# Kernel optimization log

Hardware: AMD Instinct MI355X
Metric: run time of the kernel (lower is better)

## Reference

```python
import jax, jax.numpy as jnp
import numpy as np

N_NODES = 50000
SEQ = 12
CH = 128
BS = 4

def setup_inputs() -> dict:
    key = jax.random.key(0)
    k1, k2, k3, k4, k5 = jax.random.split(key, 5)
    x = jax.random.normal(k1, (BS, N_NODES, CH), dtype=jnp.float32)
    indices = jax.random.randint(k2, (N_NODES, SEQ), 0, N_NODES)
    # xavier-uniform-like init for per-node spiral weights [n_nodes, seq]
    bound = float(np.sqrt(6.0 / (N_NODES + SEQ)))
    weight = jax.random.uniform(k3, (N_NODES, SEQ), minval=-bound, maxval=bound, dtype=jnp.float32)
    gate_w = jax.random.normal(k4, (CH, CH), dtype=jnp.float32) * (1.0 / np.sqrt(CH))
    gate_b = jax.random.normal(k5, (CH,), dtype=jnp.float32) * 0.01
    return {"x": x, "indices": indices, "weight": weight, "gate_w": gate_w, "gate_b": gate_b}

def reference(x, indices, weight, gate_w, gate_b):
    # gate projection: [bs, n, ch]
    gate = jnp.einsum('bnc,dc->bnd', x, gate_w) + gate_b
    # gather spiral neighbors along node axis: [bs, n*s, ch] -> [bs, n, s, ch]
    gathered = jnp.take(x, indices.reshape(-1), axis=1)
    gathered = gathered.reshape(x.shape[0], indices.shape[0], indices.shape[1], x.shape[2])
    # per-node weighted reduction over spiral positions
    out = jnp.einsum('bvsf,vs->bvf', gathered, weight)
    return out * gate
```

## Files before the change

kernel.cpp:

```cpp
#include <hip/hip_runtime.h>
#include <hip/hip_bf16.h>

#define N_NODES 50000
#define SEQ 12
#define CH 128
#define BS 4
#define TILE 64
#define PAD_ROW 132

typedef short bf16x8 __attribute__((ext_vector_type(8)));
typedef float f32x4 __attribute__((ext_vector_type(4)));

__global__ __launch_bounds__(256) void convert_kernel(
    const float* __restrict__ x,
    const float* __restrict__ gate_w,
    __hip_bfloat16* __restrict__ xb,
    __hip_bfloat16* __restrict__ gwb)
{
    const size_t i = (size_t)blockIdx.x * 256 + threadIdx.x;
    const size_t n8 = (size_t)BS * N_NODES * CH / 8;
    if (i < n8) {
        float4 lo = *(const float4*)(x + i * 8);
        float4 hi = *(const float4*)(x + i * 8 + 4);
        union { bf16x8 v; __hip_bfloat16 h[8]; } o;
        o.h[0] = __float2bfloat16(lo.x); o.h[1] = __float2bfloat16(lo.y);
        o.h[2] = __float2bfloat16(lo.z); o.h[3] = __float2bfloat16(lo.w);
        o.h[4] = __float2bfloat16(hi.x); o.h[5] = __float2bfloat16(hi.y);
        o.h[6] = __float2bfloat16(hi.z); o.h[7] = __float2bfloat16(hi.w);
        *(bf16x8*)((unsigned short*)xb + i * 8) = o.v;
    }
    if (i < (size_t)CH * CH / 8) {
        float4 lo = *(const float4*)(gate_w + i * 8);
        float4 hi = *(const float4*)(gate_w + i * 8 + 4);
        union { bf16x8 v; __hip_bfloat16 h[8]; } o;
        o.h[0] = __float2bfloat16(lo.x); o.h[1] = __float2bfloat16(lo.y);
        o.h[2] = __float2bfloat16(lo.z); o.h[3] = __float2bfloat16(lo.w);
        o.h[4] = __float2bfloat16(hi.x); o.h[5] = __float2bfloat16(hi.y);
        o.h[6] = __float2bfloat16(hi.z); o.h[7] = __float2bfloat16(hi.w);
        *(bf16x8*)((unsigned short*)gwb + i * 8) = o.v;
    }
}

__global__ __launch_bounds__(256) void gated_spiral_bf16_kernel(
    const __hip_bfloat16* __restrict__ xb_all,
    const int* __restrict__ indices,
    const float* __restrict__ weight,
    const __hip_bfloat16* __restrict__ gwb,
    const float* __restrict__ gate_b,
    float* __restrict__ out)
{
    __shared__ float spiral[TILE * PAD_ROW];

    const int tile = blockIdx.x;
    const int b = blockIdx.y;
    const int tid = threadIdx.x;
    const int node0 = tile * TILE;

    const unsigned short* xbb = (const unsigned short*)xb_all + (size_t)b * N_NODES * CH;

    {
        const int v = node0 + (tid >> 2);
        const int vc = v < N_NODES ? v : N_NODES - 1;
        const int q = tid & 3;

        int   idxv[SEQ];
        float wf[SEQ];
        const int*   ip = indices + (size_t)vc * SEQ;
        const float* wp = weight  + (size_t)vc * SEQ;
        #pragma unroll
        for (int s = 0; s < SEQ; ++s) {
            int t = ip[s];
            t = t < 0 ? 0 : t;
            idxv[s] = t >= N_NODES ? N_NODES - 1 : t;
            wf[s] = wp[s];
        }

        float acc[32];
        #pragma unroll
        for (int i = 0; i < 32; ++i) acc[i] = 0.f;

        #pragma unroll
        for (int s = 0; s < SEQ; ++s) {
            const unsigned short* row = xbb + (size_t)idxv[s] * CH;
            const float ws = wf[s];
            #pragma unroll
            for (int j = 0; j < 4; ++j) {
                uint4 d = *(const uint4*)(row + j * 32 + q * 8);
                unsigned int u0 = d.x, u1 = d.y, u2 = d.z, u3 = d.w;
                acc[j*8+0] += ws * __uint_as_float(u0 << 16);
                acc[j*8+1] += ws * __uint_as_float(u0 & 0xFFFF0000u);
                acc[j*8+2] += ws * __uint_as_float(u1 << 16);
                acc[j*8+3] += ws * __uint_as_float(u1 & 0xFFFF0000u);
                acc[j*8+4] += ws * __uint_as_float(u2 << 16);
                acc[j*8+5] += ws * __uint_as_float(u2 & 0xFFFF0000u);
                acc[j*8+6] += ws * __uint_as_float(u3 << 16);
                acc[j*8+7] += ws * __uint_as_float(u3 & 0xFFFF0000u);
            }
        }

        const int vl = tid >> 2;
        #pragma unroll
        for (int j = 0; j < 4; ++j) {
            float* dst = spiral + vl * PAD_ROW + j * 32 + q * 8;
            *(float4*)(dst)     = make_float4(acc[j*8+0], acc[j*8+1], acc[j*8+2], acc[j*8+3]);
            *(float4*)(dst + 4) = make_float4(acc[j*8+4], acc[j*8+5], acc[j*8+6], acc[j*8+7]);
        }
    }
    __syncthreads();

    {
        const int wave = tid >> 6;
        const int lane = tid & 63;
        const int m = lane & 15;
        const int quad = lane >> 4;

        int arow_node = node0 + wave * 16 + m;
        if (arow_node >= N_NODES) arow_node = N_NODES - 1;
        const unsigned short* ap = xbb + (size_t)arow_node * CH + quad * 8;

        bf16x8 afrag[4];
        #pragma unroll
        for (int kk = 0; kk < 4; ++kk)
            afrag[kk] = *(const bf16x8*)(ap + kk * 32);

        float gb[8];
        #pragma unroll
        for (int t = 0; t < 8; ++t)
            gb[t] = gate_b[t * 16 + m];

        const unsigned short* gw = (const unsigned short*)gwb;
        #pragma unroll
        for (int t = 0; t < 8; ++t) {
            f32x4 c = {0.f, 0.f, 0.f, 0.f};
            const unsigned short* bp = gw + (size_t)(t * 16 + m) * CH + quad * 8;
            #pragma unroll
            for (int kk = 0; kk < 4; ++kk) {
                bf16x8 bfrag = *(const bf16x8*)(bp + kk * 32);
                c = __builtin_amdgcn_mfma_f32_16x16x32_bf16(afrag[kk], bfrag, c, 0, 0, 0);
            }
            #pragma unroll
            for (int reg = 0; reg < 4; ++reg) {
                const int r = wave * 16 + quad * 4 + reg;
                const int col = t * 16 + m;
                const float sp = spiral[r * PAD_ROW + col];
                spiral[r * PAD_ROW + col] = sp * (c[reg] + gb[t]);
            }
        }
    }
    __syncthreads();

    {
        #pragma unroll
        for (int p = 0; p < 8; ++p) {
            const int seg = p * 256 + tid;
            const int row = seg >> 5;
            const int c4 = (seg & 31) * 4;
            const int node = node0 + row;
            if (node < N_NODES) {
                float4 v = *(const float4*)(spiral + row * PAD_ROW + c4);
                *(float4*)(out + ((size_t)b * N_NODES + node) * CH + c4) = v;
            }
        }
    }
}

__global__ __launch_bounds__(256) void gated_spiral_kernel(
    const float* __restrict__ x,
    const int* __restrict__ indices,
    const float* __restrict__ weight,
    const float* __restrict__ gate_w,
    const float* __restrict__ gate_b,
    float* __restrict__ out)
{
    __shared__ float spiral[TILE * PAD_ROW];

    const int tile = blockIdx.x;
    const int b = blockIdx.y;
    const int tid = threadIdx.x;
    const int node0 = tile * TILE;

    const float* xb = x + (size_t)b * N_NODES * CH;

    {
        const int v = node0 + (tid >> 2);
        const int vc = v < N_NODES ? v : N_NODES - 1;
        const int q = tid & 3;

        int   idxv[SEQ];
        float wf[SEQ];
        const int*   ip = indices + (size_t)vc * SEQ;
        const float* wp = weight  + (size_t)vc * SEQ;
        #pragma unroll
        for (int s = 0; s < SEQ; ++s) {
            int t = ip[s];
            t = t < 0 ? 0 : t;
            idxv[s] = t >= N_NODES ? N_NODES - 1 : t;
            wf[s] = wp[s];
        }

        float acc[32];
        #pragma unroll
        for (int i = 0; i < 32; ++i) acc[i] = 0.f;

        #pragma unroll
        for (int s = 0; s < SEQ; ++s) {
            const float* row = xb + (size_t)idxv[s] * CH + q * 4;
            const float ws = wf[s];
            #pragma unroll
            for (int j = 0; j < 8; ++j) {
                float4 d = *(const float4*)(row + j * 16);
                acc[j*4+0] += ws * d.x;
                acc[j*4+1] += ws * d.y;
                acc[j*4+2] += ws * d.z;
                acc[j*4+3] += ws * d.w;
            }
        }

        const int vl = tid >> 2;
        #pragma unroll
        for (int j = 0; j < 8; ++j)
            *(float4*)(spiral + vl * PAD_ROW + j * 16 + q * 4) =
                make_float4(acc[j*4+0], acc[j*4+1], acc[j*4+2], acc[j*4+3]);
    }
    __syncthreads();

    {
        const int wave = tid >> 6;
        const int lane = tid & 63;
        const int m = lane & 15;
        const int quad = lane >> 4;

        int arow_node = node0 + wave * 16 + m;
        if (arow_node >= N_NODES) arow_node = N_NODES - 1;
        const float* ap = xb + (size_t)arow_node * CH + quad * 8;

        bf16x8 afrag[4];
        #pragma unroll
        for (int kk = 0; kk < 4; ++kk) {
            float4 lo = *(const float4*)(ap + kk * 32);
            float4 hi = *(const float4*)(ap + kk * 32 + 4);
            union { bf16x8 v; __hip_bfloat16 h[8]; } af;
            af.h[0] = __float2bfloat16(lo.x); af.h[1] = __float2bfloat16(lo.y);
            af.h[2] = __float2bfloat16(lo.z); af.h[3] = __float2bfloat16(lo.w);
            af.h[4] = __float2bfloat16(hi.x); af.h[5] = __float2bfloat16(hi.y);
            af.h[6] = __float2bfloat16(hi.z); af.h[7] = __float2bfloat16(hi.w);
            afrag[kk] = af.v;
        }

        float gb[8];
        #pragma unroll
        for (int t = 0; t < 8; ++t)
            gb[t] = gate_b[t * 16 + m];

        #pragma unroll
        for (int t = 0; t < 8; ++t) {
            f32x4 c = {0.f, 0.f, 0.f, 0.f};
            const float* bp = gate_w + (size_t)(t * 16 + m) * CH + quad * 8;
            #pragma unroll
            for (int kk = 0; kk < 4; ++kk) {
                float4 lo = *(const float4*)(bp + kk * 32);
                float4 hi = *(const float4*)(bp + kk * 32 + 4);
                union { bf16x8 v; __hip_bfloat16 h[8]; } bf;
                bf.h[0] = __float2bfloat16(lo.x); bf.h[1] = __float2bfloat16(lo.y);
                bf.h[2] = __float2bfloat16(lo.z); bf.h[3] = __float2bfloat16(lo.w);
                bf.h[4] = __float2bfloat16(hi.x); bf.h[5] = __float2bfloat16(hi.y);
                bf.h[6] = __float2bfloat16(hi.z); bf.h[7] = __float2bfloat16(hi.w);
                c = __builtin_amdgcn_mfma_f32_16x16x32_bf16(afrag[kk], bf.v, c, 0, 0, 0);
            }
            #pragma unroll
            for (int reg = 0; reg < 4; ++reg) {
                const int r = wave * 16 + quad * 4 + reg;
                const int col = t * 16 + m;
                const float sp = spiral[r * PAD_ROW + col];
                spiral[r * PAD_ROW + col] = sp * (c[reg] + gb[t]);
            }
        }
    }
    __syncthreads();

    {
        #pragma unroll
        for (int p = 0; p < 8; ++p) {
            const int seg = p * 256 + tid;
            const int row = seg >> 5;
            const int c4 = (seg & 31) * 4;
            const int node = node0 + row;
            if (node < N_NODES) {
                float4 v = *(const float4*)(spiral + row * PAD_ROW + c4);
                *(float4*)(out + ((size_t)b * N_NODES + node) * CH + c4) = v;
            }
        }
    }
}

extern "C" void kernel_launch(void* const* d_in, const int* in_sizes, int n_in,
                              void* d_out, int out_size, void* d_ws, size_t ws_size,
                              hipStream_t stream) {
    const float* x       = (const float*)d_in[0];
    const int*   indices = (const int*)d_in[1];
    const float* weight  = (const float*)d_in[2];
    const float* gate_w  = (const float*)d_in[3];
    const float* gate_b  = (const float*)d_in[4];
    float*       out     = (float*)d_out;

    const size_t x_bf_bytes = (size_t)BS * N_NODES * CH * 2;
    const size_t gw_bf_bytes = (size_t)CH * CH * 2;
    dim3 grid((N_NODES + TILE - 1) / TILE, BS);

    if (ws_size >= x_bf_bytes + gw_bf_bytes) {
        __hip_bfloat16* xbuf = (__hip_bfloat16*)d_ws;
        __hip_bfloat16* gwb  = (__hip_bfloat16*)((char*)d_ws + x_bf_bytes);
        const size_t n8 = (size_t)BS * N_NODES * CH / 8;
        convert_kernel<<<dim3((unsigned)((n8 + 255) / 256)), dim3(256), 0, stream>>>(
            x, gate_w, xbuf, gwb);
        gated_spiral_bf16_kernel<<<grid, dim3(256), 0, stream>>>(
            xbuf, indices, weight, gwb, gate_b, out);
    } else {
        gated_spiral_kernel<<<grid, dim3(256), 0, stream>>>(
            x, indices, weight, gate_w, gate_b, out);
    }
}
```

Measured before the change: 345.9 us.

## Fuse bf16 conversion and spiral kernel into persistent kernel with grid barrier

```diff
diff --git a/kernel.cpp b/kernel.cpp
--- a/kernel.cpp
+++ b/kernel.cpp
@@ -7,160 +7,184 @@
 #define BS 4
 #define TILE 64
 #define PAD_ROW 132
+#define NTILES ((N_NODES + TILE - 1) / TILE)
+#define NUNITS (NTILES * BS)
 
 typedef short bf16x8 __attribute__((ext_vector_type(8)));
 typedef float f32x4 __attribute__((ext_vector_type(4)));
 
-__global__ __launch_bounds__(256) void convert_kernel(
+__device__ __forceinline__ float bflo(unsigned int u) { return __uint_as_float(u << 16); }
+__device__ __forceinline__ float bfhi(unsigned int u) { return __uint_as_float(u & 0xFFFF0000u); }
+
+__device__ unsigned int g_bar_count;
+__device__ unsigned int g_bar_gen;
+
+__device__ __forceinline__ void grid_barrier(int nblk) {
+    __syncthreads();
+    if (threadIdx.x == 0) {
+        __threadfence();
+        unsigned int gen = __hip_atomic_load(&g_bar_gen, __ATOMIC_RELAXED, __HIP_MEMORY_SCOPE_AGENT);
+        unsigned int pos = __hip_atomic_fetch_add(&g_bar_count, 1u, __ATOMIC_ACQ_REL, __HIP_MEMORY_SCOPE_AGENT);
+        if (pos == (unsigned int)(nblk - 1)) {
+            __hip_atomic_store(&g_bar_count, 0u, __ATOMIC_RELAXED, __HIP_MEMORY_SCOPE_AGENT);
+            __hip_atomic_fetch_add(&g_bar_gen, 1u, __ATOMIC_RELEASE, __HIP_MEMORY_SCOPE_AGENT);
+        } else {
+            int guard = 0;
+            while (__hip_atomic_load(&g_bar_gen, __ATOMIC_ACQUIRE, __HIP_MEMORY_SCOPE_AGENT) == gen) {
+                __builtin_amdgcn_s_sleep(2);
+                if (++guard > (1 << 22)) break;
+            }
+        }
+    }
+    __syncthreads();
+    __threadfence();
+}
+
+__global__ __launch_bounds__(256, 4) void fused_gated_spiral(
     const float* __restrict__ x,
-    const float* __restrict__ gate_w,
-    __hip_bfloat16* __restrict__ xb,
-    __hip_bfloat16* __restrict__ gwb)
-{
-    const size_t i = (size_t)blockIdx.x * 256 + threadIdx.x;
-    const size_t n8 = (size_t)BS * N_NODES * CH / 8;
-    if (i < n8) {
-        float4 lo = *(const float4*)(x + i * 8);
-        float4 hi = *(const float4*)(x + i * 8 + 4);
-        union { bf16x8 v; __hip_bfloat16 h[8]; } o;
-        o.h[0] = __float2bfloat16(lo.x); o.h[1] = __float2bfloat16(lo.y);
-        o.h[2] = __float2bfloat16(lo.z); o.h[3] = __float2bfloat16(lo.w);
-        o.h[4] = __float2bfloat16(hi.x); o.h[5] = __float2bfloat16(hi.y);
-        o.h[6] = __float2bfloat16(hi.z); o.h[7] = __float2bfloat16(hi.w);
-        *(bf16x8*)((unsigned short*)xb + i * 8) = o.v;
-    }
-    if (i < (size_t)CH * CH / 8) {
-        float4 lo = *(const float4*)(gate_w + i * 8);
-        float4 hi = *(const float4*)(gate_w + i * 8 + 4);
-        union { bf16x8 v; __hip_bfloat16 h[8]; } o;
-        o.h[0] = __float2bfloat16(lo.x); o.h[1] = __float2bfloat16(lo.y);
-        o.h[2] = __float2bfloat16(lo.z); o.h[3] = __float2bfloat16(lo.w);
-        o.h[4] = __float2bfloat16(hi.x); o.h[5] = __float2bfloat16(hi.y);
-        o.h[6] = __float2bfloat16(hi.z); o.h[7] = __float2bfloat16(hi.w);
-        *(bf16x8*)((unsigned short*)gwb + i * 8) = o.v;
-    }
-}
-
-__global__ __launch_bounds__(256) void gated_spiral_bf16_kernel(
-    const __hip_bfloat16* __restrict__ xb_all,
     const int* __restrict__ indices,
     const float* __restrict__ weight,
-    const __hip_bfloat16* __restrict__ gwb,
+    const float* __restrict__ gate_w,
     const float* __restrict__ gate_b,
-    float* __restrict__ out)
+    unsigned short* __restrict__ xb,
+    unsigned short* __restrict__ gwb,
+    float* __restrict__ out,
+    int nblk)
 {
     __shared__ float spiral[TILE * PAD_ROW];
-
-    const int tile = blockIdx.x;
-    const int b = blockIdx.y;
+    __shared__ int   idx_s[TILE * SEQ];
+    __shared__ float w_s[TILE * SEQ];
+
     const int tid = threadIdx.x;
-    const int node0 = tile * TILE;
-
-    const unsigned short* xbb = (const unsigned short*)xb_all + (size_t)b * N_NODES * CH;
 
     {
-        const int v = node0 + (tid >> 2);
-        const int vc = v < N_NODES ? v : N_NODES - 1;
-        const int q = tid & 3;
-
-        int   idxv[SEQ];
-        float wf[SEQ];
-        const int*   ip = indices + (size_t)vc * SEQ;
-        const float* wp = weight  + (size_t)vc * SEQ;
-        #pragma unroll
-        for (int s = 0; s < SEQ; ++s) {
-            int t = ip[s];
-            t = t < 0 ? 0 : t;
-            idxv[s] = t >= N_NODES ? N_NODES - 1 : t;
-            wf[s] = wp[s];
-        }
-
-        float acc[32];
-        #pragma unroll
-        for (int i = 0; i < 32; ++i) acc[i] = 0.f;
-
-        #pragma unroll
-        for (int s = 0; s < SEQ; ++s) {
-            const unsigned short* row = xbb + (size_t)idxv[s] * CH;
-            const float ws = wf[s];
-            #pragma unroll
-            for (int j = 0; j < 4; ++j) {
-                uint4 d = *(const uint4*)(row + j * 32 + q * 8);
-                unsigned int u0 = d.x, u1 = d.y, u2 = d.z, u3 = d.w;
-                acc[j*8+0] += ws * __uint_as_float(u0 << 16);
-                acc[j*8+1] += ws * __uint_as_float(u0 & 0xFFFF0000u);
-                acc[j*8+2] += ws * __uint_as_float(u1 << 16);
-                acc[j*8+3] += ws * __uint_as_float(u1 & 0xFFFF0000u);
-                acc[j*8+4] += ws * __uint_as_float(u2 << 16);
-                acc[j*8+5] += ws * __uint_as_float(u2 & 0xFFFF0000u);
-                acc[j*8+6] += ws * __uint_as_float(u3 << 16);
-                acc[j*8+7] += ws * __uint_as_float(u3 & 0xFFFF0000u);
-            }
-        }
-
-        const int vl = tid >> 2;
-        #pragma unroll
-        for (int j = 0; j < 4; ++j) {
-            float* dst = spiral + vl * PAD_ROW + j * 32 + q * 8;
-            *(float4*)(dst)     = make_float4(acc[j*8+0], acc[j*8+1], acc[j*8+2], acc[j*8+3]);
-            *(float4*)(dst + 4) = make_float4(acc[j*8+4], acc[j*8+5], acc[j*8+6], acc[j*8+7]);
-        }
-    }
-    __syncthreads();
-
-    {
-        const int wave = tid >> 6;
-        const int lane = tid & 63;
-        const int m = lane & 15;
-        const int quad = lane >> 4;
-
-        int arow_node = node0 + wave * 16 + m;
-        if (arow_node >= N_NODES) arow_node = N_NODES - 1;
-        const unsigned short* ap = xbb + (size_t)arow_node * CH + quad * 8;
-
-        bf16x8 afrag[4];
-        #pragma unroll
-        for (int kk = 0; kk < 4; ++kk)
-            afrag[kk] = *(const bf16x8*)(ap + kk * 32);
-
-        float gb[8];
-        #pragma unroll
-        for (int t = 0; t < 8; ++t)
-            gb[t] = gate_b[t * 16 + m];
-
-        const unsigned short* gw = (const unsigned short*)gwb;
-        #pragma unroll
-        for (int t = 0; t < 8; ++t) {
-            f32x4 c = {0.f, 0.f, 0.f, 0.f};
-            const unsigned short* bp = gw + (size_t)(t * 16 + m) * CH + quad * 8;
-            #pragma unroll
-            for (int kk = 0; kk < 4; ++kk) {
-                bf16x8 bfrag = *(const bf16x8*)(bp + kk * 32);
-                c = __builtin_amdgcn_mfma_f32_16x16x32_bf16(afrag[kk], bfrag, c, 0, 0, 0);
-            }
-            #pragma unroll
-            for (int reg = 0; reg < 4; ++reg) {
-                const int r = wave * 16 + quad * 4 + reg;
-                const int col = t * 16 + m;
-                const float sp = spiral[r * PAD_ROW + col];
-                spiral[r * PAD_ROW + col] = sp * (c[reg] + gb[t]);
-            }
-        }
-    }
-    __syncthreads();
-
-    {
-        #pragma unroll
-        for (int p = 0; p < 8; ++p) {
-            const int seg = p * 256 + tid;
-            const int row = seg >> 5;
-            const int c4 = (seg & 31) * 4;
-            const int node = node0 + row;
-            if (node < N_NODES) {
-                float4 v = *(const float4*)(spiral + row * PAD_ROW + c4);
-                *(float4*)(out + ((size_t)b * N_NODES + node) * CH + c4) = v;
-            }
-        }
+        const size_t n8 = (size_t)BS * N_NODES * CH / 8;
+        const size_t stride = (size_t)nblk * 256;
+        for (size_t i = (size_t)blockIdx.x * 256 + tid; i < n8; i += stride) {
+            float4 lo = *(const float4*)(x + i * 8);
+            float4 hi = *(const float4*)(x + i * 8 + 4);
+            union { bf16x8 v; __hip_bfloat16 h[8]; } o;
+            o.h[0] = __float2bfloat16(lo.x); o.h[1] = __float2bfloat16(lo.y);
+            o.h[2] = __float2bfloat16(lo.z); o.h[3] = __float2bfloat16(lo.w);
+            o.h[4] = __float2bfloat16(hi.x); o.h[5] = __float2bfloat16(hi.y);
+            o.h[6] = __float2bfloat16(hi.z); o.h[7] = __float2bfloat16(hi.w);
+            *(bf16x8*)(xb + i * 8) = o.v;
+        }
+        const size_t g0 = (size_t)blockIdx.x * 256 + tid;
+        if (g0 < (size_t)CH * CH / 8) {
+            float4 lo = *(const float4*)(gate_w + g0 * 8);
+            float4 hi = *(const float4*)(gate_w + g0 * 8 + 4);
+            union { bf16x8 v; __hip_bfloat16 h[8]; } o;
+            o.h[0] = __float2bfloat16(lo.x); o.h[1] = __float2bfloat16(lo.y);
+            o.h[2] = __float2bfloat16(lo.z); o.h[3] = __float2bfloat16(lo.w);
+            o.h[4] = __float2bfloat16(hi.x); o.h[5] = __float2bfloat16(hi.y);
+            o.h[6] = __float2bfloat16(hi.z); o.h[7] = __float2bfloat16(hi.w);
+            *(bf16x8*)(gwb + g0 * 8) = o.v;
+        }
+    }
+    grid_barrier(nblk);
+
+    for (int unit = blockIdx.x; unit < NUNITS; unit += nblk) {
+        const int tile = unit >> 2;
+        const int b = unit & 3;
+        const int node0 = tile * TILE;
+        const unsigned short* xbb = xb + (size_t)b * N_NODES * CH;
+
+        for (int k = tid; k < TILE * SEQ; k += 256) {
+            int node = node0 + k / SEQ;
+            if (node >= N_NODES) node = N_NODES - 1;
+            int t = indices[(size_t)node * SEQ + (k % SEQ)];
+            t = t < 0 ? 0 : (t >= N_NODES ? N_NODES - 1 : t);
+            idx_s[k] = t;
+            w_s[k] = weight[(size_t)node * SEQ + (k % SEQ)];
+        }
+        __syncthreads();
+
+        {
+            const int c0 = (tid & 15) * 8;
+            const int rbase = tid >> 4;
+            #pragma unroll 2
+            for (int g = 0; g < 4; ++g) {
+                const int r = g * 16 + rbase;
+                int us[SEQ]; float wv[SEQ];
+                #pragma unroll
+                for (int s = 0; s < SEQ; ++s) {
+                    us[s] = idx_s[r * SEQ + s];
+                    wv[s] = w_s[r * SEQ + s];
+                }
+                float acc[8];
+                #pragma unroll
+                for (int i = 0; i < 8; ++i) acc[i] = 0.f;
+                #pragma unroll
+                for (int s = 0; s < SEQ; ++s) {
+                    const uint4 d = *(const uint4*)(xbb + (size_t)us[s] * CH + c0);
+                    const float ws = wv[s];
+                    acc[0] += ws * bflo(d.x); acc[1] += ws * bfhi(d.x);
+                    acc[2] += ws * bflo(d.y); acc[3] += ws * bfhi(d.y);
+                    acc[4] += ws * bflo(d.z); acc[5] += ws * bfhi(d.z);
+                    acc[6] += ws * bflo(d.w); acc[7] += ws * bfhi(d.w);
+                }
+                float* dst = spiral + r * PAD_ROW + c0;
+                *(float4*)(dst)     = make_float4(acc[0], acc[1], acc[2], acc[3]);
+                *(float4*)(dst + 4) = make_float4(acc[4], acc[5], acc[6], acc[7]);
+            }
+        }
+        __syncthreads();
+
+        {
+            const int wave = tid >> 6;
+            const int lane = tid & 63;
+            const int m = lane & 15;
+            const int quad = lane >> 4;
+
+            int arow_node = node0 + wave * 16 + m;
+            if (arow_node >= N_NODES) arow_node = N_NODES - 1;
+            const unsigned short* ap = xbb + (size_t)arow_node * CH + quad * 8;
+
+            bf16x8 afrag[4];
+            #pragma unroll
+            for (int kk = 0; kk < 4; ++kk)
+                afrag[kk] = *(const bf16x8*)(ap + kk * 32);
+
+            float gb[8];
+            #pragma unroll
+            for (int t = 0; t < 8; ++t)
+                gb[t] = gate_b[t * 16 + m];
+
+            #pragma unroll
+            for (int t = 0; t < 8; ++t) {
+                f32x4 c = {0.f, 0.f, 0.f, 0.f};
+                const unsigned short* bp = gwb + (size_t)(t * 16 + m) * CH + quad * 8;
+                #pragma unroll
+                for (int kk = 0; kk < 4; ++kk) {
+                    bf16x8 bfrag = *(const bf16x8*)(bp + kk * 32);
+                    c = __builtin_amdgcn_mfma_f32_16x16x32_bf16(afrag[kk], bfrag, c, 0, 0, 0);
+                }
+                #pragma unroll
+                for (int reg = 0; reg < 4; ++reg) {
+                    const int r = wave * 16 + quad * 4 + reg;
+                    const int col = t * 16 + m;
+                    const float sp = spiral[r * PAD_ROW + col];
+                    spiral[r * PAD_ROW + col] = sp * (c[reg] + gb[t]);
+                }
+            }
+        }
+        __syncthreads();
+
+        {
+            #pragma unroll
+            for (int p = 0; p < 8; ++p) {
+                const int seg = p * 256 + tid;
+                const int row = seg >> 5;
+                const int c4 = (seg & 31) * 4;
+                const int node = node0 + row;
+                if (node < N_NODES) {
+                    float4 v = *(const float4*)(spiral + row * PAD_ROW + c4);
+                    *(float4*)(out + ((size_t)b * N_NODES + node) * CH + c4) = v;
+                }
+            }
+        }
+        __syncthreads();
     }
 }
 
@@ -303,19 +327,26 @@
     const float* gate_b  = (const float*)d_in[4];
     float*       out     = (float*)d_out;
 
-    const size_t x_bf_bytes = (size_t)BS * N_NODES * CH * 2;
+    const size_t x_bf_bytes  = (size_t)BS * N_NODES * CH * 2;
     const size_t gw_bf_bytes = (size_t)CH * CH * 2;
-    dim3 grid((N_NODES + TILE - 1) / TILE, BS);
 
     if (ws_size >= x_bf_bytes + gw_bf_bytes) {
-        __hip_bfloat16* xbuf = (__hip_bfloat16*)d_ws;
-        __hip_bfloat16* gwb  = (__hip_bfloat16*)((char*)d_ws + x_bf_bytes);
-        const size_t n8 = (size_t)BS * N_NODES * CH / 8;
-        convert_kernel<<<dim3((unsigned)((n8 + 255) / 256)), dim3(256), 0, stream>>>(
-            x, gate_w, xbuf, gwb);
-        gated_spiral_bf16_kernel<<<grid, dim3(256), 0, stream>>>(
-            xbuf, indices, weight, gwb, gate_b, out);
+        unsigned short* xbuf = (unsigned short*)d_ws;
+        unsigned short* gwb  = (unsigned short*)((char*)d_ws + x_bf_bytes);
+
+        static int s_nblk = 0;
+        if (s_nblk == 0) {
+            int per_cu = 0;
+            hipError_t e = hipOccupancyMaxActiveBlocksPerMultiprocessor(
+                &per_cu, fused_gated_spiral, 256, 0);
+            if (e != hipSuccess || per_cu < 1) per_cu = 1;
+            if (per_cu > 4) per_cu = 4;
+            s_nblk = per_cu * 256;
+        }
+        fused_gated_spiral<<<dim3(s_nblk), dim3(256), 0, stream>>>(
+            x, indices, weight, gate_w, gate_b, xbuf, gwb, out, s_nblk);
     } else {
+        dim3 grid((N_NODES + TILE - 1) / TILE, BS);
         gated_spiral_kernel<<<grid, dim3(256), 0, stream>>>(
             x, indices, weight, gate_w, gate_b, out);
     }
```

Result: slower. 585.4 us (+69.2%).

## Replace bf16 pre-convert path with async global-to-LDS double-buffered gather kernel

Applied to the files above, without the earlier changes.

```diff
diff --git a/kernel.cpp b/kernel.cpp
--- a/kernel.cpp
+++ b/kernel.cpp
@@ -7,164 +7,24 @@
 #define BS 4
 #define TILE 64
 #define PAD_ROW 132
+#define NTILES ((N_NODES + TILE - 1) / TILE)
+
+#define NODES_PER_WAVE 16
+#define CHUNK_NODES 2
+#define CHUNK_FLOATS (CHUNK_NODES * SEQ * CH)
+#define NCHUNK (NODES_PER_WAVE / CHUNK_NODES)
 
 typedef short bf16x8 __attribute__((ext_vector_type(8)));
 typedef float f32x4 __attribute__((ext_vector_type(4)));
 
-__global__ __launch_bounds__(256) void convert_kernel(
-    const float* __restrict__ x,
-    const float* __restrict__ gate_w,
-    __hip_bfloat16* __restrict__ xb,
-    __hip_bfloat16* __restrict__ gwb)
-{
-    const size_t i = (size_t)blockIdx.x * 256 + threadIdx.x;
-    const size_t n8 = (size_t)BS * N_NODES * CH / 8;
-    if (i < n8) {
-        float4 lo = *(const float4*)(x + i * 8);
-        float4 hi = *(const float4*)(x + i * 8 + 4);
-        union { bf16x8 v; __hip_bfloat16 h[8]; } o;
-        o.h[0] = __float2bfloat16(lo.x); o.h[1] = __float2bfloat16(lo.y);
-        o.h[2] = __float2bfloat16(lo.z); o.h[3] = __float2bfloat16(lo.w);
-        o.h[4] = __float2bfloat16(hi.x); o.h[5] = __float2bfloat16(hi.y);
-        o.h[6] = __float2bfloat16(hi.z); o.h[7] = __float2bfloat16(hi.w);
-        *(bf16x8*)((unsigned short*)xb + i * 8) = o.v;
-    }
-    if (i < (size_t)CH * CH / 8) {
-        float4 lo = *(const float4*)(gate_w + i * 8);
-        float4 hi = *(const float4*)(gate_w + i * 8 + 4);
-        union { bf16x8 v; __hip_bfloat16 h[8]; } o;
-        o.h[0] = __float2bfloat16(lo.x); o.h[1] = __float2bfloat16(lo.y);
-        o.h[2] = __float2bfloat16(lo.z); o.h[3] = __float2bfloat16(lo.w);
-        o.h[4] = __float2bfloat16(hi.x); o.h[5] = __float2bfloat16(hi.y);
-        o.h[6] = __float2bfloat16(hi.z); o.h[7] = __float2bfloat16(hi.w);
-        *(bf16x8*)((unsigned short*)gwb + i * 8) = o.v;
-    }
+__device__ __forceinline__ void gload_lds16(const float* g, float* l) {
+    __builtin_amdgcn_global_load_lds(
+        (const __attribute__((address_space(1))) void*)g,
+        (__attribute__((address_space(3))) void*)l,
+        16, 0, 0);
 }
 
-__global__ __launch_bounds__(256) void gated_spiral_bf16_kernel(
-    const __hip_bfloat16* __restrict__ xb_all,
-    const int* __restrict__ indices,
-    const float* __restrict__ weight,
-    const __hip_bfloat16* __restrict__ gwb,
-    const float* __restrict__ gate_b,
-    float* __restrict__ out)
-{
-    __shared__ float spiral[TILE * PAD_ROW];
-
-    const int tile = blockIdx.x;
-    const int b = blockIdx.y;
-    const int tid = threadIdx.x;
-    const int node0 = tile * TILE;
-
-    const unsigned short* xbb = (const unsigned short*)xb_all + (size_t)b * N_NODES * CH;
-
-    {
-        const int v = node0 + (tid >> 2);
-        const int vc = v < N_NODES ? v : N_NODES - 1;
-        const int q = tid & 3;
-
-        int   idxv[SEQ];
-        float wf[SEQ];
-        const int*   ip = indices + (size_t)vc * SEQ;
-        const float* wp = weight  + (size_t)vc * SEQ;
-        #pragma unroll
-        for (int s = 0; s < SEQ; ++s) {
-            int t = ip[s];
-            t = t < 0 ? 0 : t;
-            idxv[s] = t >= N_NODES ? N_NODES - 1 : t;
-            wf[s] = wp[s];
-        }
-
-        float acc[32];
-        #pragma unroll
-        for (int i = 0; i < 32; ++i) acc[i] = 0.f;
-
-        #pragma unroll
-        for (int s = 0; s < SEQ; ++s) {
-            const unsigned short* row = xbb + (size_t)idxv[s] * CH;
-            const float ws = wf[s];
-            #pragma unroll
-            for (int j = 0; j < 4; ++j) {
-                uint4 d = *(const uint4*)(row + j * 32 + q * 8);
-                unsigned int u0 = d.x, u1 = d.y, u2 = d.z, u3 = d.w;
-                acc[j*8+0] += ws * __uint_as_float(u0 << 16);
-                acc[j*8+1] += ws * __uint_as_float(u0 & 0xFFFF0000u);
-                acc[j*8+2] += ws * __uint_as_float(u1 << 16);
-                acc[j*8+3] += ws * __uint_as_float(u1 & 0xFFFF0000u);
-                acc[j*8+4] += ws * __uint_as_float(u2 << 16);
-                acc[j*8+5] += ws * __uint_as_float(u2 & 0xFFFF0000u);
-                acc[j*8+6] += ws * __uint_as_float(u3 << 16);
-                acc[j*8+7] += ws * __uint_as_float(u3 & 0xFFFF0000u);
-            }
-        }
-
-        const int vl = tid >> 2;
-        #pragma unroll
-        for (int j = 0; j < 4; ++j) {
-            float* dst = spiral + vl * PAD_ROW + j * 32 + q * 8;
-            *(float4*)(dst)     = make_float4(acc[j*8+0], acc[j*8+1], acc[j*8+2], acc[j*8+3]);
-            *(float4*)(dst + 4) = make_float4(acc[j*8+4], acc[j*8+5], acc[j*8+6], acc[j*8+7]);
-        }
-    }
-    __syncthreads();
-
-    {
-        const int wave = tid >> 6;
-        const int lane = tid & 63;
-        const int m = lane & 15;
-        const int quad = lane >> 4;
-
-        int arow_node = node0 + wave * 16 + m;
-        if (arow_node >= N_NODES) arow_node = N_NODES - 1;
-        const unsigned short* ap = xbb + (size_t)arow_node * CH + quad * 8;
-
-        bf16x8 afrag[4];
-        #pragma unroll
-        for (int kk = 0; kk < 4; ++kk)
-            afrag[kk] = *(const bf16x8*)(ap + kk * 32);
-
-        float gb[8];
-        #pragma unroll
-        for (int t = 0; t < 8; ++t)
-            gb[t] = gate_b[t * 16 + m];
-
-        const unsigned short* gw = (const unsigned short*)gwb;
-        #pragma unroll
-        for (int t = 0; t < 8; ++t) {
-            f32x4 c = {0.f, 0.f, 0.f, 0.f};
-            const unsigned short* bp = gw + (size_t)(t * 16 + m) * CH + quad * 8;
-            #pragma unroll
-            for (int kk = 0; kk < 4; ++kk) {
-                bf16x8 bfrag = *(const bf16x8*)(bp + kk * 32);
-                c = __builtin_amdgcn_mfma_f32_16x16x32_bf16(afrag[kk], bfrag, c, 0, 0, 0);
-            }
-            #pragma unroll
-            for (int reg = 0; reg < 4; ++reg) {
-                const int r = wave * 16 + quad * 4 + reg;
-                const int col = t * 16 + m;
-                const float sp = spiral[r * PAD_ROW + col];
-                spiral[r * PAD_ROW + col] = sp * (c[reg] + gb[t]);
-            }
-        }
-    }
-    __syncthreads();
-
-    {
-        #pragma unroll
-        for (int p = 0; p < 8; ++p) {
-            const int seg = p * 256 + tid;
-            const int row = seg >> 5;
-            const int c4 = (seg & 31) * 4;
-            const int node = node0 + row;
-            if (node < N_NODES) {
-                float4 v = *(const float4*)(spiral + row * PAD_ROW + c4);
-                *(float4*)(out + ((size_t)b * N_NODES + node) * CH + c4) = v;
-            }
-        }
-    }
-}
-
-__global__ __launch_bounds__(256) void gated_spiral_kernel(
+__global__ __launch_bounds__(256, 1) void gated_spiral_async(
     const float* __restrict__ x,
     const int* __restrict__ indices,
     const float* __restrict__ weight,
@@ -173,60 +33,79 @@
     float* __restrict__ out)
 {
     __shared__ float spiral[TILE * PAD_ROW];
+    __shared__ float gbuf[4][2][CHUNK_FLOATS];
+    __shared__ int   idx_s[TILE * SEQ];
+    __shared__ float w_s[TILE * SEQ];
 
-    const int tile = blockIdx.x;
-    const int b = blockIdx.y;
-    const int tid = threadIdx.x;
-    const int node0 = tile * TILE;
-
+    const int tid  = threadIdx.x;
+    const int wave = tid >> 6;
+    const int lane = tid & 63;
+    const int b    = blockIdx.y;
+    const int node0 = blockIdx.x * TILE;
     const float* xb = x + (size_t)b * N_NODES * CH;
 
+    const int sbase = wave * NODES_PER_WAVE * SEQ;
+    #pragma unroll
+    for (int k3 = 0; k3 < 3; ++k3) {
+        const int k = k3 * 64 + lane;
+        int node = node0 + wave * NODES_PER_WAVE + k / SEQ;
+        if (node >= N_NODES) node = N_NODES - 1;
+        int t = indices[(size_t)node * SEQ + (k % SEQ)];
+        t = t < 0 ? 0 : (t >= N_NODES ? N_NODES - 1 : t);
+        idx_s[sbase + k] = t;
+        w_s[sbase + k]   = weight[(size_t)node * SEQ + (k % SEQ)];
+    }
+
     {
-        const int v = node0 + (tid >> 2);
-        const int vc = v < N_NODES ? v : N_NODES - 1;
-        const int q = tid & 3;
-
-        int   idxv[SEQ];
-        float wf[SEQ];
-        const int*   ip = indices + (size_t)vc * SEQ;
-        const float* wp = weight  + (size_t)vc * SEQ;
-        #pragma unroll
-        for (int s = 0; s < SEQ; ++s) {
-            int t = ip[s];
-            t = t < 0 ? 0 : t;
-            idxv[s] = t >= N_NODES ? N_NODES - 1 : t;
-            wf[s] = wp[s];
-        }
-
-        float acc[32];
-        #pragma unroll
-        for (int i = 0; i < 32; ++i) acc[i] = 0.f;
+        const int n  = lane >> 5;
+        const int co = (lane & 31) * 4;
+        const int* idxw = idx_s + sbase;
+        const float* ww = w_s + sbase;
+        float* gb0 = &gbuf[wave][0][0];
 
         #pragma unroll
-        for (int s = 0; s < SEQ; ++s) {
-            const float* row = xb + (size_t)idxv[s] * CH + q * 4;
-            const float ws = wf[s];
+        for (int c0 = 0; c0 < 2; ++c0) {
+            const int* ix = idxw + c0 * CHUNK_NODES * SEQ;
+            float* dst = gb0 + c0 * CHUNK_FLOATS;
             #pragma unroll
-            for (int j = 0; j < 8; ++j) {
-                float4 d = *(const float4*)(row + j * 16);
-                acc[j*4+0] += ws * d.x;
-                acc[j*4+1] += ws * d.y;
-                acc[j*4+2] += ws * d.z;
-                acc[j*4+3] += ws * d.w;
+            for (int s = 0; s < SEQ; ++s) {
+                const int row = ix[n * SEQ + s];
+                gload_lds16(xb + (size_t)row * CH + co, dst + s * (CHUNK_NODES * CH));
             }
         }
 
-        const int vl = tid >> 2;
         #pragma unroll
-        for (int j = 0; j < 8; ++j)
-            *(float4*)(spiral + vl * PAD_ROW + j * 16 + q * 4) =
-                make_float4(acc[j*4+0], acc[j*4+1], acc[j*4+2], acc[j*4+3]);
+        for (int c = 0; c < NCHUNK; ++c) {
+            if (c < NCHUNK - 1) asm volatile("s_waitcnt vmcnt(12)" ::: "memory");
+            else                asm volatile("s_waitcnt vmcnt(0)"  ::: "memory");
+            __builtin_amdgcn_sched_barrier(0);
+
+            float* cur = gb0 + (c & 1) * CHUNK_FLOATS;
+            const float* wp = ww + c * CHUNK_NODES * SEQ + n * SEQ;
+            float a0 = 0.f, a1 = 0.f, a2 = 0.f, a3 = 0.f;
+            #pragma unroll
+            for (int s = 0; s < SEQ; ++s) {
+                const float4 d = *(const float4*)(cur + (s * CHUNK_NODES + n) * CH + co);
+                const float ws = wp[s];
+                a0 += ws * d.x; a1 += ws * d.y; a2 += ws * d.z; a3 += ws * d.w;
+            }
+            const int r = wave * NODES_PER_WAVE + c * CHUNK_NODES + n;
+            *(float4*)(spiral + r * PAD_ROW + co) = make_float4(a0, a1, a2, a3);
+
+            if (c + 2 < NCHUNK) {
+                asm volatile("s_waitcnt lgkmcnt(0)" ::: "memory");
+                __builtin_amdgcn_sched_barrier(0);
+                const int* ix = idxw + (c + 2) * CHUNK_NODES * SEQ;
+                #pragma unroll
+                for (int s = 0; s < SEQ; ++s) {
+                    const int row = ix[n * SEQ + s];
+                    gload_lds16(xb + (size_t)row * CH + co, cur + s * (CHUNK_NODES * CH));
+                }
+            }
+        }
     }
-    __syncthreads();
 
     {
-        const int wave = tid >> 6;
-        const int lane = tid & 63;
         const int m = lane & 15;
         const int quad = lane >> 4;
 
@@ -247,10 +126,10 @@
             afrag[kk] = af.v;
         }
 
-        float gb[8];
+        float gbv[8];
         #pragma unroll
         for (int t = 0; t < 8; ++t)
-            gb[t] = gate_b[t * 16 + m];
+            gbv[t] = gate_b[t * 16 + m];
 
         #pragma unroll
         for (int t = 0; t < 8; ++t) {
@@ -272,22 +151,22 @@
                 const int r = wave * 16 + quad * 4 + reg;
                 const int col = t * 16 + m;
                 const float sp = spiral[r * PAD_ROW + col];
-                spiral[r * PAD_ROW + col] = sp * (c[reg] + gb[t]);
+                spiral[r * PAD_ROW + col] = sp * (c[reg] + gbv[t]);
             }
         }
     }
-    __syncthreads();
 
     {
         #pragma unroll
         for (int p = 0; p < 8; ++p) {
-            const int seg = p * 256 + tid;
-            const int row = seg >> 5;
+            const int seg = p * 64 + lane;
+            const int r = seg >> 5;
             const int c4 = (seg & 31) * 4;
-            const int node = node0 + row;
+            const int node = node0 + wave * 16 + r;
             if (node < N_NODES) {
-                float4 v = *(const float4*)(spiral + row * PAD_ROW + c4);
-                *(float4*)(out + ((size_t)b * N_NODES + node) * CH + c4) = v;
+                const float* sp = spiral + (wave * 16 + r) * PAD_ROW + c4;
+                f32x4 v = { sp[0], sp[1], sp[2], sp[3] };
+                __builtin_nontemporal_store(v, (f32x4*)(out + ((size_t)b * N_NODES + node) * CH + c4));
             }
         }
     }
@@ -303,20 +182,7 @@
     const float* gate_b  = (const float*)d_in[4];
     float*       out     = (float*)d_out;
 
-    const size_t x_bf_bytes = (size_t)BS * N_NODES * CH * 2;
-    const size_t gw_bf_bytes = (size_t)CH * CH * 2;
-    dim3 grid((N_NODES + TILE - 1) / TILE, BS);
-
-    if (ws_size >= x_bf_bytes + gw_bf_bytes) {
-        __hip_bfloat16* xbuf = (__hip_bfloat16*)d_ws;
-        __hip_bfloat16* gwb  = (__hip_bfloat16*)((char*)d_ws + x_bf_bytes);
-        const size_t n8 = (size_t)BS * N_NODES * CH / 8;
-        convert_kernel<<<dim3((unsigned)((n8 + 255) / 256)), dim3(256), 0, stream>>>(
-            x, gate_w, xbuf, gwb);
-        gated_spiral_bf16_kernel<<<grid, dim3(256), 0, stream>>>(
-            xbuf, indices, weight, gwb, gate_b, out);
-    } else {
-        gated_spiral_kernel<<<grid, dim3(256), 0, stream>>>(
-            x, indices, weight, gate_w, gate_b, out);
-    }
+    dim3 grid(NTILES, BS);
+    gated_spiral_async<<<grid, dim3(256), 0, stream>>>(
+        x, indices, weight, gate_w, gate_b, out);
 }
```

Measured after the change: 400.4 us. 15.8% more time.
